# Kernel tuning notes

Measured on AMD Instinct MI355X. Metric: run time of the kernel, lower is better.

## Reference

```python
import jax, jax.numpy as jnp
import numpy as np

B, N, FIN, FOUT = 8, 1024, 512, 256
ALPHA = 0.2      # LeakyReLU negative slope
EPS = 1e-5       # LayerNorm eps
NEG = -9e15      # mask value


def setup_inputs() -> dict:
    key = jax.random.key(0)
    k_h, k_adj, k_W, k_a, k_g, k_b = jax.random.split(key, 6)
    h = jax.random.normal(k_h, (B, N, FIN), dtype=jnp.float32)
    # sparse-ish binary adjacency (float, as in the torch module: adj > 0 masks)
    adj = jax.random.bernoulli(k_adj, p=0.1, shape=(B, N, N)).astype(jnp.float32)
    # xavier_uniform with gain=1.414
    def xavier(k, shape, gain=1.414):
        fan_in, fan_out = shape[0], shape[1]
        lim = gain * np.sqrt(6.0 / (fan_in + fan_out))
        return jax.random.uniform(k, shape, jnp.float32, -lim, lim)
    W = xavier(k_W, (FIN, FOUT))
    a = xavier(k_a, (2 * FOUT, 1))
    ln_gamma = jnp.ones((FOUT,), jnp.float32)
    ln_beta = jnp.zeros((FOUT,), jnp.float32)
    return {"h": h, "adj": adj, "q_type": 0, "pos": 0,
            "W": W, "a": a, "ln_gamma": ln_gamma, "ln_beta": ln_beta}


def reference(h, adj, q_type, pos, W, a, ln_gamma, ln_beta):
    # h: [B,N,FIN], adj: [B,N,N]
    Wh = jnp.einsum('bnf,fo->bno', h, W)              # [B,N,FOUT]
    # a^T [Wh_i || Wh_j] decomposes into per-node terms (same math as the
    # torch repeat/cat construction, without the [B,N,N,2F] blowup)
    a1, a2 = a[:FOUT, 0], a[FOUT:, 0]                 # [FOUT], [FOUT]
    f1 = Wh @ a1                                      # [B,N] (source i)
    f2 = Wh @ a2                                      # [B,N] (target j)
    e = jax.nn.leaky_relu(f1[:, :, None] + f2[:, None, :], negative_slope=ALPHA)
    e = jnp.where(adj > 0, e, NEG)
    attention = jax.nn.softmax(e, axis=2)             # [B,N,N]
    # dropout is a no-op at inference (training=False)
    h_prime = jnp.einsum('bij,bjo->bio', attention, Wh)  # [B,N,FOUT]
    mu = jnp.mean(h_prime, axis=-1, keepdims=True)
    var = jnp.var(h_prime, axis=-1, keepdims=True)
    h_norm = (h_prime - mu) * jax.lax.rsqrt(var + EPS) * ln_gamma + ln_beta
    return jax.nn.gelu(h_norm, approximate=False)     # concat=True -> gelu
```

## Files before the change

kernel.cpp:

```cpp
#include <hip/hip_runtime.h>
#include <math.h>

#define B_    8
#define N_    1024
#define FIN   512
#define FOUT  256
#define ALPHA 0.2f
#define EPSV  1e-5f

typedef __attribute__((ext_vector_type(8))) short bf16x8;
typedef __attribute__((ext_vector_type(4))) float f32x4;

__device__ __forceinline__ short f2bf(float x) {
    unsigned u = __builtin_bit_cast(unsigned, x);
    u = (u + 0x7FFFu + ((u >> 16) & 1u)) >> 16;
    return (short)u;
}
__device__ __forceinline__ short f2bf_fast(float x) {
    unsigned u = __builtin_bit_cast(unsigned, x);
    return (short)((u + 0x8000u) >> 16);
}
__device__ __forceinline__ float bf2f(short s) {
    return __builtin_bit_cast(float, ((unsigned)(unsigned short)s) << 16);
}
__device__ __forceinline__ float gelu_exact(float x) {
    return 0.5f * x * (1.0f + erff(x * 0.70710678118654752f));
}


__global__ __launch_bounds__(256) void k_prep(const float* __restrict__ W,
                                              short* __restrict__ WT) {
    int id  = blockIdx.x * 256 + threadIdx.x;
    int col = id >> 7;
    int k4  = (id & 127) * 4;
    short4 v;
    v.x = f2bf(W[(k4 + 0) * FOUT + col]);
    v.y = f2bf(W[(k4 + 1) * FOUT + col]);
    v.z = f2bf(W[(k4 + 2) * FOUT + col]);
    v.w = f2bf(W[(k4 + 3) * FOUT + col]);
    *(short4*)(WT + (long)col * FIN + k4) = v;
}

__global__ __launch_bounds__(256) void k_bits(const float* __restrict__ adj,
                                              unsigned char* __restrict__ bits) {
    const int tid = threadIdx.x;
    const int w   = tid >> 6, l = tid & 63;
    const long gr = (long)blockIdx.x * 4 + w;
    const float* __restrict__ arow = adj + gr * N_;

    unsigned b0 = 0, b1 = 0;
    {
        float4 x0 = *(const float4*)(arow + l * 8);
        float4 x1 = *(const float4*)(arow + l * 8 + 4);
        float aa[8] = {x0.x, x0.y, x0.z, x0.w, x1.x, x1.y, x1.z, x1.w};
        #pragma unroll
        for (int u = 0; u < 8; ++u) b0 |= (aa[u] > 0.f ? 1u : 0u) << u;
        float4 y0 = *(const float4*)(arow + 512 + l * 8);
        float4 y1 = *(const float4*)(arow + 512 + l * 8 + 4);
        float bb[8] = {y0.x, y0.y, y0.z, y0.w, y1.x, y1.y, y1.z, y1.w};
        #pragma unroll
        for (int u = 0; u < 8; ++u) b1 |= (bb[u] > 0.f ? 1u : 0u) << u;
    }
    unsigned out2 = 0;
    #pragma unroll
    for (int k = 0; k < 2; ++k) {
        int o   = 2 * l + k;
        int lqd = o >> 5, ktd = o & 31;
        int src = ((ktd & 15) << 2) | lqd;
        unsigned v0 = __shfl(b0, src, 64);
        unsigned v1 = __shfl(b1, src, 64);
        unsigned v  = (ktd & 16) ? v1 : v0;
        out2 |= (v & 0xFFu) << (8 * k);
    }
    *(unsigned short*)(bits + gr * 128 + l * 2) = (unsigned short)out2;
}

__global__ __launch_bounds__(256) void k_wh(const float* __restrict__ h,
                                            const short* __restrict__ WT,
                                            const float* __restrict__ a,
                                            short* __restrict__ Bpack,
                                            float* __restrict__ F1,
                                            float* __restrict__ F2) {
    const int tid = threadIdx.x;
    const int w   = tid >> 6, l = tid & 63;
    const int lr  = l & 15, lq = l >> 4;
    const long row0 = (long)blockIdx.x * 16;
    const int colbase = w * 64;

    __shared__ float r1[4][16], r2[4][16];

    f32x4 acc[4] = {};
    const float* hrow = h + (row0 + lr) * FIN + lq * 8;

    #pragma unroll
    for (int k0 = 0; k0 < FIN; k0 += 32) {
        float4 v0 = *(const float4*)(hrow + k0);
        float4 v1 = *(const float4*)(hrow + k0 + 4);
        bf16x8 af;
        af[0] = f2bf(v0.x); af[1] = f2bf(v0.y); af[2] = f2bf(v0.z); af[3] = f2bf(v0.w);
        af[4] = f2bf(v1.x); af[5] = f2bf(v1.y); af[6] = f2bf(v1.z); af[7] = f2bf(v1.w);
        #pragma unroll
        for (int c = 0; c < 4; ++c) {
            const short* bp = WT + (long)(colbase + c * 16 + lr) * FIN + k0 + lq * 8;
            bf16x8 bf = *(const bf16x8*)bp;
            acc[c] = __builtin_amdgcn_mfma_f32_16x16x32_bf16(af, bf, acc[c], 0, 0, 0);
        }
    }

    const int b   = (int)(row0 >> 10);
    const int il0 = (int)(row0 & 1023);
    const int kt  = il0 >> 5;
    const int h16 = (il0 >> 4) & 1;
    const int lp  = (h16 * 2 + (lq >> 1)) * 16 + lr;
    const int u0  = (lq & 1) * 4;
    short* bpo = Bpack + ((long)b * 16 * 32) * 512;
    #pragma unroll
    for (int c = 0; c < 4; ++c) {
        short4 s;
        s.x = f2bf(acc[c][0]); s.y = f2bf(acc[c][1]);
        s.z = f2bf(acc[c][2]); s.w = f2bf(acc[c][3]);
        int n16 = w * 4 + c;
        *(short4*)(bpo + ((long)(n16 * 32 + kt)) * 512 + lp * 8 + u0) = s;
    }

    float p1[4] = {0.f, 0.f, 0.f, 0.f}, p2[4] = {0.f, 0.f, 0.f, 0.f};
    #pragma unroll
    for (int c = 0; c < 4; ++c) {
        int col = colbase + c * 16 + lr;
        float a1v = a[col], a2v = a[FOUT + col];
        #pragma unroll
        for (int j = 0; j < 4; ++j) { p1[j] += acc[c][j] * a1v; p2[j] += acc[c][j] * a2v; }
    }
    #pragma unroll
    for (int off = 1; off < 16; off <<= 1) {
        #pragma unroll
        for (int j = 0; j < 4; ++j) {
            p1[j] += __shfl_xor(p1[j], off, 64);
            p2[j] += __shfl_xor(p2[j], off, 64);
        }
    }
    if (lr == 0) {
        #pragma unroll
        for (int j = 0; j < 4; ++j) { r1[w][lq * 4 + j] = p1[j]; r2[w][lq * 4 + j] = p2[j]; }
    }
    __syncthreads();
    if (tid < 16) {
        F1[row0 + tid] = r1[0][tid] + r1[1][tid] + r1[2][tid] + r1[3][tid];
        F2[row0 + tid] = r2[0][tid] + r2[1][tid] + r2[2][tid] + r2[3][tid];
    }
}

__global__ __launch_bounds__(256) void k_pv(const short* __restrict__ Bpack,
                                            const unsigned char* __restrict__ bits,
                                            const float* __restrict__ F1,
                                            const float* __restrict__ F2,
                                            const float* __restrict__ gamma,
                                            const float* __restrict__ beta,
                                            float* __restrict__ out) {
    const int tid = threadIdx.x;
    const int b   = blockIdx.x;
    const int i0  = blockIdx.y * 16;
    const int w   = tid >> 6, l = tid & 63;
    const int lr  = l & 15, lq = l >> 4;

    __shared__ float f2s[N_];
    __shared__ float lnp1[4][16], lnp2[4][16];

    { int j = tid * 4; *(float4*)&f2s[j] = *(const float4*)(F2 + b * N_ + j); }
    __syncthreads();

    const float f1 = F1[b * N_ + i0 + lr];
    unsigned bw[8];
    {
        const unsigned char* pb = bits + ((long)(b * N_ + i0 + lr)) * 128 + lq * 32;
        uint4 q0 = *(const uint4*)pb;
        uint4 q1 = *(const uint4*)(pb + 16);
        bw[0]=q0.x; bw[1]=q0.y; bw[2]=q0.z; bw[3]=q0.w;
        bw[4]=q1.x; bw[5]=q1.y; bw[6]=q1.z; bw[7]=q1.w;
    }
    const short* __restrict__ bp = Bpack + (((long)b * 16 + w * 4) * 32) * 512 + l * 8;

    f32x4 acc[4] = {};
    float ls = 0.f;

    bf16x8 bc0 = *(const bf16x8*)(bp);
    bf16x8 bc1 = *(const bf16x8*)(bp + 32 * 512);
    bf16x8 bc2 = *(const bf16x8*)(bp + 64 * 512);
    bf16x8 bc3 = *(const bf16x8*)(bp + 96 * 512);

    #pragma unroll
    for (int t = 0; t < 32; ++t) {
        bf16x8 bn0 = bc0, bn1 = bc1, bn2 = bc2, bn3 = bc3;
        if (t < 31) {
            bn0 = *(const bf16x8*)(bp + (t + 1) * 512);
            bn1 = *(const bf16x8*)(bp + (32 + t + 1) * 512);
            bn2 = *(const bf16x8*)(bp + (64 + t + 1) * 512);
            bn3 = *(const bf16x8*)(bp + (96 + t + 1) * 512);
        }
        float f2k[8];
        *(float4*)&f2k[0] = *(const float4*)&f2s[t * 32 + lq * 8];
        *(float4*)&f2k[4] = *(const float4*)&f2s[t * 32 + lq * 8 + 4];
        const unsigned byte = (bw[t >> 2] >> ((t & 3) * 8)) & 0xFFu;

        bf16x8 af;
        #pragma unroll
        for (int u = 0; u < 8; ++u) {
            float x  = f1 + f2k[u];
            float tt = fmaxf(x, ALPHA * x);
            float e  = ((byte >> u) & 1u) ? __expf(tt) : 0.f;
            short s  = f2bf_fast(e);
            af[u] = s;
            ls += bf2f(s);
        }
        acc[0] = __builtin_amdgcn_mfma_f32_16x16x32_bf16(af, bc0, acc[0], 0, 0, 0);
        acc[1] = __builtin_amdgcn_mfma_f32_16x16x32_bf16(af, bc1, acc[1], 0, 0, 0);
        acc[2] = __builtin_amdgcn_mfma_f32_16x16x32_bf16(af, bc2, acc[2], 0, 0, 0);
        acc[3] = __builtin_amdgcn_mfma_f32_16x16x32_bf16(af, bc3, acc[3], 0, 0, 0);
        bc0 = bn0; bc1 = bn1; bc2 = bn2; bc3 = bn3;
    }

    ls += __shfl_xor(ls, 16, 64);
    ls += __shfl_xor(ls, 32, 64);
    float il[4];
    #pragma unroll
    for (int jj = 0; jj < 4; ++jj) {
        float r = __shfl(ls, lq * 4 + jj, 64);
        il[jj] = (r > 0.f) ? 1.0f / r : 0.f;
    }

    float s1[4] = {0.f,0.f,0.f,0.f}, s2[4] = {0.f,0.f,0.f,0.f};
    #pragma unroll
    for (int cf = 0; cf < 4; ++cf)
        #pragma unroll
        for (int jj = 0; jj < 4; ++jj) {
            float v = acc[cf][jj] * il[jj];
            acc[cf][jj] = v;
            s1[jj] += v;
            s2[jj] += v * v;
        }
    #pragma unroll
    for (int off = 1; off < 16; off <<= 1)
        #pragma unroll
        for (int jj = 0; jj < 4; ++jj) {
            s1[jj] += __shfl_xor(s1[jj], off, 64);
            s2[jj] += __shfl_xor(s2[jj], off, 64);
        }
    if (lr == 0) {
        #pragma unroll
        for (int jj = 0; jj < 4; ++jj) {
            lnp1[w][lq * 4 + jj] = s1[jj];
            lnp2[w][lq * 4 + jj] = s2[jj];
        }
    }
    __syncthreads();

    #pragma unroll
    for (int jj = 0; jj < 4; ++jj) {
        int row = lq * 4 + jj;
        float t1 = lnp1[0][row] + lnp1[1][row] + lnp1[2][row] + lnp1[3][row];
        float t2 = lnp2[0][row] + lnp2[1][row] + lnp2[2][row] + lnp2[3][row];
        float mu   = t1 * (1.0f / FOUT);
        float rstd = rsqrtf(t2 * (1.0f / FOUT) - mu * mu + EPSV);
        #pragma unroll
        for (int cf = 0; cf < 4; ++cf) {
            int col = w * 64 + cf * 16 + lr;
            out[((long)b * N_ + i0 + row) * FOUT + col] =
                gelu_exact((acc[cf][jj] - mu) * rstd * gamma[col] + beta[col]);
        }
    }
}

extern "C" void kernel_launch(void* const* d_in, const int* in_sizes, int n_in,
                              void* d_out, int out_size, void* d_ws, size_t ws_size,
                              hipStream_t stream) {
    const float* h     = (const float*)d_in[0];
    const float* adj   = (const float*)d_in[1];
    const float* W     = (const float*)d_in[4];
    const float* a     = (const float*)d_in[5];
    const float* gamma = (const float*)d_in[6];
    const float* beta  = (const float*)d_in[7];
    float* out = (float*)d_out;

    short* Bpack = (short*)d_ws;
    short* WT    = Bpack + (size_t)B_ * 16 * 32 * 512;
    float* F1    = (float*)(WT + (size_t)FOUT * FIN);
    float* F2    = F1 + (size_t)B_ * N_;
    unsigned char* bits = (unsigned char*)(F2 + (size_t)B_ * N_);

    k_prep<<<dim3(128), 256, 0, stream>>>(W, WT);
    k_bits<<<dim3(B_ * N_ / 4), 256, 0, stream>>>(adj, bits);
    k_wh  <<<dim3(B_ * N_ / 16), 256, 0, stream>>>(h, WT, a, Bpack, F1, F2);
    k_pv  <<<dim3(B_, N_ / 16), 256, 0, stream>>>(Bpack, bits, F1, F2, gamma, beta, out);
}
```

Before: 60.33 us.

## Split k_pv reduction dimension across two wave groups with LDS combine

Doubles the k_pv block to 512 threads so two groups of four waves each cover half of the key dimension. Partial accumulators and row sums are combined through shared memory before LayerNorm and GELU. The explicit software prefetch of B operands is dropped in favour of direct loads, leaving latency hiding to the extra waves. The intent is to halve the serial MFMA/exp chain per wave and raise occupancy. The cost is extra LDS traffic, another barrier, and half the waves idling during the epilogue.

```diff
diff --git a/kernel.cpp b/kernel.cpp
--- a/kernel.cpp
+++ b/kernel.cpp
@@ -150,56 +150,47 @@
     }
 }
 
-__global__ __launch_bounds__(256) void k_pv(const short* __restrict__ Bpack,
-                                            const unsigned char* __restrict__ bits,
-                                            const float* __restrict__ F1,
-                                            const float* __restrict__ F2,
-                                            const float* __restrict__ gamma,
-                                            const float* __restrict__ beta,
-                                            float* __restrict__ out) {
+__global__ __launch_bounds__(512, 4) void k_pv(const short* __restrict__ Bpack,
+                                               const unsigned char* __restrict__ bits,
+                                               const float* __restrict__ F1,
+                                               const float* __restrict__ F2,
+                                               const float* __restrict__ gamma,
+                                               const float* __restrict__ beta,
+                                               float* __restrict__ out) {
     const int tid = threadIdx.x;
     const int b   = blockIdx.x;
     const int i0  = blockIdx.y * 16;
     const int w   = tid >> 6, l = tid & 63;
     const int lr  = l & 15, lq = l >> 4;
+    const int cw  = w & 3;
+    const int kg  = w >> 2;
 
     __shared__ float f2s[N_];
+    __shared__ float sc[4][16][68];
     __shared__ float lnp1[4][16], lnp2[4][16];
-
-    { int j = tid * 4; *(float4*)&f2s[j] = *(const float4*)(F2 + b * N_ + j); }
+    __shared__ float lsumS[2][16];
+
+    { int j = tid * 2; *(float2*)&f2s[j] = *(const float2*)(F2 + b * N_ + j); }
     __syncthreads();
 
     const float f1 = F1[b * N_ + i0 + lr];
-    unsigned bw[8];
+    unsigned bw[4];
     {
-        const unsigned char* pb = bits + ((long)(b * N_ + i0 + lr)) * 128 + lq * 32;
-        uint4 q0 = *(const uint4*)pb;
-        uint4 q1 = *(const uint4*)(pb + 16);
-        bw[0]=q0.x; bw[1]=q0.y; bw[2]=q0.z; bw[3]=q0.w;
-        bw[4]=q1.x; bw[5]=q1.y; bw[6]=q1.z; bw[7]=q1.w;
-    }
-    const short* __restrict__ bp = Bpack + (((long)b * 16 + w * 4) * 32) * 512 + l * 8;
+        const unsigned char* pb = bits + ((long)(b * N_ + i0 + lr)) * 128 + lq * 32 + kg * 16;
+        uint4 q = *(const uint4*)pb;
+        bw[0] = q.x; bw[1] = q.y; bw[2] = q.z; bw[3] = q.w;
+    }
+    const short* __restrict__ bp =
+        Bpack + (((long)b * 16 + cw * 4) * 32 + kg * 16) * 512 + l * 8;
 
     f32x4 acc[4] = {};
     float ls = 0.f;
 
-    bf16x8 bc0 = *(const bf16x8*)(bp);
-    bf16x8 bc1 = *(const bf16x8*)(bp + 32 * 512);
-    bf16x8 bc2 = *(const bf16x8*)(bp + 64 * 512);
-    bf16x8 bc3 = *(const bf16x8*)(bp + 96 * 512);
-
-    #pragma unroll
-    for (int t = 0; t < 32; ++t) {
-        bf16x8 bn0 = bc0, bn1 = bc1, bn2 = bc2, bn3 = bc3;
-        if (t < 31) {
-            bn0 = *(const bf16x8*)(bp + (t + 1) * 512);
-            bn1 = *(const bf16x8*)(bp + (32 + t + 1) * 512);
-            bn2 = *(const bf16x8*)(bp + (64 + t + 1) * 512);
-            bn3 = *(const bf16x8*)(bp + (96 + t + 1) * 512);
-        }
+    #pragma unroll
+    for (int t = 0; t < 16; ++t) {
         float f2k[8];
-        *(float4*)&f2k[0] = *(const float4*)&f2s[t * 32 + lq * 8];
-        *(float4*)&f2k[4] = *(const float4*)&f2s[t * 32 + lq * 8 + 4];
+        *(float4*)&f2k[0] = *(const float4*)&f2s[(kg * 16 + t) * 32 + lq * 8];
+        *(float4*)&f2k[4] = *(const float4*)&f2s[(kg * 16 + t) * 32 + lq * 8 + 4];
         const unsigned byte = (bw[t >> 2] >> ((t & 3) * 8)) & 0xFFu;
 
         bf16x8 af;
@@ -212,60 +203,83 @@
             af[u] = s;
             ls += bf2f(s);
         }
-        acc[0] = __builtin_amdgcn_mfma_f32_16x16x32_bf16(af, bc0, acc[0], 0, 0, 0);
-        acc[1] = __builtin_amdgcn_mfma_f32_16x16x32_bf16(af, bc1, acc[1], 0, 0, 0);
-        acc[2] = __builtin_amdgcn_mfma_f32_16x16x32_bf16(af, bc2, acc[2], 0, 0, 0);
-        acc[3] = __builtin_amdgcn_mfma_f32_16x16x32_bf16(af, bc3, acc[3], 0, 0, 0);
-        bc0 = bn0; bc1 = bn1; bc2 = bn2; bc3 = bn3;
+        bf16x8 b0 = *(const bf16x8*)(bp + (long)t * 512);
+        bf16x8 b1 = *(const bf16x8*)(bp + (long)(32 + t) * 512);
+        bf16x8 b2 = *(const bf16x8*)(bp + (long)(64 + t) * 512);
+        bf16x8 b3 = *(const bf16x8*)(bp + (long)(96 + t) * 512);
+        acc[0] = __builtin_amdgcn_mfma_f32_16x16x32_bf16(af, b0, acc[0], 0, 0, 0);
+        acc[1] = __builtin_amdgcn_mfma_f32_16x16x32_bf16(af, b1, acc[1], 0, 0, 0);
+        acc[2] = __builtin_amdgcn_mfma_f32_16x16x32_bf16(af, b2, acc[2], 0, 0, 0);
+        acc[3] = __builtin_amdgcn_mfma_f32_16x16x32_bf16(af, b3, acc[3], 0, 0, 0);
     }
 
     ls += __shfl_xor(ls, 16, 64);
     ls += __shfl_xor(ls, 32, 64);
-    float il[4];
-    #pragma unroll
-    for (int jj = 0; jj < 4; ++jj) {
-        float r = __shfl(ls, lq * 4 + jj, 64);
-        il[jj] = (r > 0.f) ? 1.0f / r : 0.f;
-    }
-
-    float s1[4] = {0.f,0.f,0.f,0.f}, s2[4] = {0.f,0.f,0.f,0.f};
-    #pragma unroll
-    for (int cf = 0; cf < 4; ++cf)
+    if (cw == 0 && lq == 0) lsumS[kg][lr] = ls;
+
+    if (kg == 1) {
+        #pragma unroll
+        for (int cf = 0; cf < 4; ++cf)
+            #pragma unroll
+            for (int jj = 0; jj < 4; ++jj)
+                sc[cw][lq * 4 + jj][cf * 16 + lr] = acc[cf][jj];
+    }
+    __syncthreads();
+
+    if (kg == 0) {
+        #pragma unroll
+        for (int cf = 0; cf < 4; ++cf)
+            #pragma unroll
+            for (int jj = 0; jj < 4; ++jj)
+                acc[cf][jj] += sc[cw][lq * 4 + jj][cf * 16 + lr];
+
+        float il[4];
         #pragma unroll
         for (int jj = 0; jj < 4; ++jj) {
-            float v = acc[cf][jj] * il[jj];
-            acc[cf][jj] = v;
-            s1[jj] += v;
-            s2[jj] += v * v;
-        }
-    #pragma unroll
-    for (int off = 1; off < 16; off <<= 1)
+            float r = lsumS[0][lq * 4 + jj] + lsumS[1][lq * 4 + jj];
+            il[jj] = (r > 0.f) ? 1.0f / r : 0.f;
+        }
+        float s1[4] = {0.f,0.f,0.f,0.f}, s2[4] = {0.f,0.f,0.f,0.f};
+        #pragma unroll
+        for (int cf = 0; cf < 4; ++cf)
+            #pragma unroll
+            for (int jj = 0; jj < 4; ++jj) {
+                float v = acc[cf][jj] * il[jj];
+                acc[cf][jj] = v;
+                s1[jj] += v;
+                s2[jj] += v * v;
+            }
+        #pragma unroll
+        for (int off = 1; off < 16; off <<= 1)
+            #pragma unroll
+            for (int jj = 0; jj < 4; ++jj) {
+                s1[jj] += __shfl_xor(s1[jj], off, 64);
+                s2[jj] += __shfl_xor(s2[jj], off, 64);
+            }
+        if (lr == 0) {
+            #pragma unroll
+            for (int jj = 0; jj < 4; ++jj) {
+                lnp1[cw][lq * 4 + jj] = s1[jj];
+                lnp2[cw][lq * 4 + jj] = s2[jj];
+            }
+        }
+    }
+    __syncthreads();
+
+    if (kg == 0) {
         #pragma unroll
         for (int jj = 0; jj < 4; ++jj) {
-            s1[jj] += __shfl_xor(s1[jj], off, 64);
-            s2[jj] += __shfl_xor(s2[jj], off, 64);
-        }
-    if (lr == 0) {
-        #pragma unroll
-        for (int jj = 0; jj < 4; ++jj) {
-            lnp1[w][lq * 4 + jj] = s1[jj];
-            lnp2[w][lq * 4 + jj] = s2[jj];
-        }
-    }
-    __syncthreads();
-
-    #pragma unroll
-    for (int jj = 0; jj < 4; ++jj) {
-        int row = lq * 4 + jj;
-        float t1 = lnp1[0][row] + lnp1[1][row] + lnp1[2][row] + lnp1[3][row];
-        float t2 = lnp2[0][row] + lnp2[1][row] + lnp2[2][row] + lnp2[3][row];
-        float mu   = t1 * (1.0f / FOUT);
-        float rstd = rsqrtf(t2 * (1.0f / FOUT) - mu * mu + EPSV);
-        #pragma unroll
-        for (int cf = 0; cf < 4; ++cf) {
-            int col = w * 64 + cf * 16 + lr;
-            out[((long)b * N_ + i0 + row) * FOUT + col] =
-                gelu_exact((acc[cf][jj] - mu) * rstd * gamma[col] + beta[col]);
+            int row = lq * 4 + jj;
+            float t1 = lnp1[0][row] + lnp1[1][row] + lnp1[2][row] + lnp1[3][row];
+            float t2 = lnp2[0][row] + lnp2[1][row] + lnp2[2][row] + lnp2[3][row];
+            float mu   = t1 * (1.0f / FOUT);
+            float rstd = rsqrtf(t2 * (1.0f / FOUT) - mu * mu + EPSV);
+            #pragma unroll
+            for (int cf = 0; cf < 4; ++cf) {
+                int col = cw * 64 + cf * 16 + lr;
+                out[((long)b * N_ + i0 + row) * FOUT + col] =
+                    gelu_exact((acc[cf][jj] - mu) * rstd * gamma[col] + beta[col]);
+            }
         }
     }
 }
@@ -290,5 +304,5 @@
     k_prep<<<dim3(128), 256, 0, stream>>>(W, WT);
     k_bits<<<dim3(B_ * N_ / 4), 256, 0, stream>>>(adj, bits);
     k_wh  <<<dim3(B_ * N_ / 16), 256, 0, stream>>>(h, WT, a, Bpack, F1, F2);
-    k_pv  <<<dim3(B_, N_ / 16), 256, 0, stream>>>(Bpack, bits, F1, F2, gamma, beta, out);
-}
+    k_pv  <<<dim3(B_, N_ / 16), 512, 0, stream>>>(Bpack, bits, F1, F2, gamma, beta, out);
+}
```

Measured after the change: 60.43 us. No clear change (+0.2%).

## Split attention into prob-gen, LDS-staged MFMA GEMM, and separate LayerNorm kernels

Applied to the files above, without the earlier changes.

The fused attention kernel is split into three kernels. k_pgen materializes the masked exp scores as packed bf16 A tiles plus row sums. k_pv is a double-buffered GEMM that stages A and B tiles into LDS with global_load_lds and computes 32x128 output tiles. k_ln then applies the softmax normalization, LayerNorm and GELU in place. The aim is more reuse of Wh tiles across rows and better MFMA throughput, at the cost of writing and re-reading a 16MB bf16 probability matrix and the fp32 intermediate, plus two extra launches.

```diff
diff --git a/kernel.cpp b/kernel.cpp
--- a/kernel.cpp
+++ b/kernel.cpp
@@ -150,124 +150,169 @@
     }
 }
 
-__global__ __launch_bounds__(256) void k_pv(const short* __restrict__ Bpack,
-                                            const unsigned char* __restrict__ bits,
-                                            const float* __restrict__ F1,
-                                            const float* __restrict__ F2,
-                                            const float* __restrict__ gamma,
-                                            const float* __restrict__ beta,
-                                            float* __restrict__ out) {
+__global__ __launch_bounds__(256) void k_pgen(const unsigned char* __restrict__ bits,
+                                              const float* __restrict__ F1,
+                                              const float* __restrict__ F2,
+                                              short* __restrict__ Apack,
+                                              float* __restrict__ lrow) {
     const int tid = threadIdx.x;
     const int b   = blockIdx.x;
-    const int i0  = blockIdx.y * 16;
+    const int m16 = blockIdx.y;
+    const int i0  = m16 * 16;
     const int w   = tid >> 6, l = tid & 63;
     const int lr  = l & 15, lq = l >> 4;
 
     __shared__ float f2s[N_];
-    __shared__ float lnp1[4][16], lnp2[4][16];
-
+    __shared__ float lred[4][16];
     { int j = tid * 4; *(float4*)&f2s[j] = *(const float4*)(F2 + b * N_ + j); }
     __syncthreads();
 
     const float f1 = F1[b * N_ + i0 + lr];
-    unsigned bw[8];
-    {
-        const unsigned char* pb = bits + ((long)(b * N_ + i0 + lr)) * 128 + lq * 32;
-        uint4 q0 = *(const uint4*)pb;
-        uint4 q1 = *(const uint4*)(pb + 16);
-        bw[0]=q0.x; bw[1]=q0.y; bw[2]=q0.z; bw[3]=q0.w;
-        bw[4]=q1.x; bw[5]=q1.y; bw[6]=q1.z; bw[7]=q1.w;
-    }
-    const short* __restrict__ bp = Bpack + (((long)b * 16 + w * 4) * 32) * 512 + l * 8;
-
-    f32x4 acc[4] = {};
+    const uint2 bw2 = *(const uint2*)(bits + ((long)(b * N_ + i0 + lr)) * 128 + lq * 32 + w * 8);
+    const unsigned bwv[2] = {bw2.x, bw2.y};
+    short* __restrict__ apb = Apack + (((long)b * 64 + m16) * 32) * 512;
+
     float ls = 0.f;
-
-    bf16x8 bc0 = *(const bf16x8*)(bp);
-    bf16x8 bc1 = *(const bf16x8*)(bp + 32 * 512);
-    bf16x8 bc2 = *(const bf16x8*)(bp + 64 * 512);
-    bf16x8 bc3 = *(const bf16x8*)(bp + 96 * 512);
-
-    #pragma unroll
-    for (int t = 0; t < 32; ++t) {
-        bf16x8 bn0 = bc0, bn1 = bc1, bn2 = bc2, bn3 = bc3;
-        if (t < 31) {
-            bn0 = *(const bf16x8*)(bp + (t + 1) * 512);
-            bn1 = *(const bf16x8*)(bp + (32 + t + 1) * 512);
-            bn2 = *(const bf16x8*)(bp + (64 + t + 1) * 512);
-            bn3 = *(const bf16x8*)(bp + (96 + t + 1) * 512);
-        }
+    #pragma unroll
+    for (int it = 0; it < 8; ++it) {
+        const int kt = w * 8 + it;
+        const unsigned byte = (bwv[it >> 2] >> ((it & 3) * 8)) & 0xFFu;
         float f2k[8];
-        *(float4*)&f2k[0] = *(const float4*)&f2s[t * 32 + lq * 8];
-        *(float4*)&f2k[4] = *(const float4*)&f2s[t * 32 + lq * 8 + 4];
-        const unsigned byte = (bw[t >> 2] >> ((t & 3) * 8)) & 0xFFu;
-
-        bf16x8 af;
+        *(float4*)&f2k[0] = *(const float4*)&f2s[kt * 32 + lq * 8];
+        *(float4*)&f2k[4] = *(const float4*)&f2s[kt * 32 + lq * 8 + 4];
+        bf16x8 pv;
         #pragma unroll
         for (int u = 0; u < 8; ++u) {
             float x  = f1 + f2k[u];
             float tt = fmaxf(x, ALPHA * x);
             float e  = ((byte >> u) & 1u) ? __expf(tt) : 0.f;
             short s  = f2bf_fast(e);
-            af[u] = s;
+            pv[u] = s;
             ls += bf2f(s);
         }
-        acc[0] = __builtin_amdgcn_mfma_f32_16x16x32_bf16(af, bc0, acc[0], 0, 0, 0);
-        acc[1] = __builtin_amdgcn_mfma_f32_16x16x32_bf16(af, bc1, acc[1], 0, 0, 0);
-        acc[2] = __builtin_amdgcn_mfma_f32_16x16x32_bf16(af, bc2, acc[2], 0, 0, 0);
-        acc[3] = __builtin_amdgcn_mfma_f32_16x16x32_bf16(af, bc3, acc[3], 0, 0, 0);
-        bc0 = bn0; bc1 = bn1; bc2 = bn2; bc3 = bn3;
+        *(bf16x8*)(apb + (long)kt * 512 + l * 8) = pv;
     }
 
     ls += __shfl_xor(ls, 16, 64);
     ls += __shfl_xor(ls, 32, 64);
-    float il[4];
-    #pragma unroll
-    for (int jj = 0; jj < 4; ++jj) {
-        float r = __shfl(ls, lq * 4 + jj, 64);
-        il[jj] = (r > 0.f) ? 1.0f / r : 0.f;
-    }
-
-    float s1[4] = {0.f,0.f,0.f,0.f}, s2[4] = {0.f,0.f,0.f,0.f};
-    #pragma unroll
-    for (int cf = 0; cf < 4; ++cf)
-        #pragma unroll
-        for (int jj = 0; jj < 4; ++jj) {
-            float v = acc[cf][jj] * il[jj];
-            acc[cf][jj] = v;
-            s1[jj] += v;
-            s2[jj] += v * v;
-        }
-    #pragma unroll
-    for (int off = 1; off < 16; off <<= 1)
-        #pragma unroll
-        for (int jj = 0; jj < 4; ++jj) {
-            s1[jj] += __shfl_xor(s1[jj], off, 64);
-            s2[jj] += __shfl_xor(s2[jj], off, 64);
-        }
-    if (lr == 0) {
-        #pragma unroll
-        for (int jj = 0; jj < 4; ++jj) {
-            lnp1[w][lq * 4 + jj] = s1[jj];
-            lnp2[w][lq * 4 + jj] = s2[jj];
-        }
-    }
+    if (lq == 0) lred[w][lr] = ls;
     __syncthreads();
-
-    #pragma unroll
-    for (int jj = 0; jj < 4; ++jj) {
-        int row = lq * 4 + jj;
-        float t1 = lnp1[0][row] + lnp1[1][row] + lnp1[2][row] + lnp1[3][row];
-        float t2 = lnp2[0][row] + lnp2[1][row] + lnp2[2][row] + lnp2[3][row];
-        float mu   = t1 * (1.0f / FOUT);
-        float rstd = rsqrtf(t2 * (1.0f / FOUT) - mu * mu + EPSV);
-        #pragma unroll
-        for (int cf = 0; cf < 4; ++cf) {
-            int col = w * 64 + cf * 16 + lr;
-            out[((long)b * N_ + i0 + row) * FOUT + col] =
-                gelu_exact((acc[cf][jj] - mu) * rstd * gamma[col] + beta[col]);
-        }
-    }
+    if (tid < 16)
+        lrow[(long)b * N_ + i0 + tid] = lred[0][tid] + lred[1][tid] + lred[2][tid] + lred[3][tid];
+}
+
+__global__ __launch_bounds__(128) void k_pv(const short* __restrict__ Apack,
+                                            const short* __restrict__ Bpack,
+                                            float* __restrict__ hp) {
+    const int tid = threadIdx.x;
+    const int w   = tid >> 6, l = tid & 63;
+    const int lr  = l & 15, lq = l >> 4;
+    const int rg  = ((blockIdx.x & 7) << 5) | (blockIdx.x >> 3);
+    const int b   = rg >> 5;
+    const int rloc= rg & 31;
+    const int cg  = blockIdx.y;
+
+    __shared__ short sbuf[2][20 * 512];
+
+    const short* __restrict__ abase = Apack + (((long)b * 64 + rloc * 2) * 32) * 512 + (long)l * 8;
+    const short* __restrict__ bbase = Bpack + (((long)b * 16 + cg * 8) * 32) * 512 + (long)l * 8;
+
+    f32x4 acc[2][4] = {};
+
+    auto stage = [&](int buf, int t) {
+        const int kt0 = t * 2;
+        #pragma unroll
+        for (int c = w; c < 20; c += 2) {
+            const short* src;
+            if (c < 4) {
+                src = abase + ((long)(c >> 1) * 32 + kt0 + (c & 1)) * 512;
+            } else {
+                int idx = c - 4;
+                src = bbase + ((long)(idx >> 1) * 32 + kt0 + (idx & 1)) * 512;
+            }
+            __builtin_amdgcn_global_load_lds(
+                (const __attribute__((address_space(1))) unsigned int*)src,
+                (__attribute__((address_space(3))) unsigned int*)&sbuf[buf][c * 512],
+                16, 0, 0);
+        }
+    };
+
+    auto compute = [&](int buf) {
+        #pragma unroll
+        for (int kt2 = 0; kt2 < 2; ++kt2) {
+            bf16x8 a0 = *(const bf16x8*)&sbuf[buf][(0 + kt2) * 512 + l * 8];
+            bf16x8 a1 = *(const bf16x8*)&sbuf[buf][(2 + kt2) * 512 + l * 8];
+            #pragma unroll
+            for (int cf = 0; cf < 4; ++cf) {
+                const int n = w * 4 + cf;
+                bf16x8 bv = *(const bf16x8*)&sbuf[buf][(4 + n * 2 + kt2) * 512 + l * 8];
+                acc[0][cf] = __builtin_amdgcn_mfma_f32_16x16x32_bf16(a0, bv, acc[0][cf], 0, 0, 0);
+                acc[1][cf] = __builtin_amdgcn_mfma_f32_16x16x32_bf16(a1, bv, acc[1][cf], 0, 0, 0);
+            }
+        }
+    };
+
+    stage(0, 0);
+    __syncthreads();
+    int cur = 0;
+    for (int t = 0; t < 16; ++t) {
+        if (t < 15) stage(cur ^ 1, t + 1);
+        compute(cur);
+        __syncthreads();
+        cur ^= 1;
+    }
+
+    const long row0 = (long)b * 1024 + (long)rloc * 32;
+    const int  c0   = cg * 128 + w * 64;
+    #pragma unroll
+    for (int rf = 0; rf < 2; ++rf)
+        #pragma unroll
+        for (int cf = 0; cf < 4; ++cf)
+            #pragma unroll
+            for (int jj = 0; jj < 4; ++jj)
+                hp[(row0 + rf * 16 + lq * 4 + jj) * FOUT + c0 + cf * 16 + lr] = acc[rf][cf][jj];
+}
+
+__global__ __launch_bounds__(256) void k_ln(float* __restrict__ hp,
+                                            const float* __restrict__ lrow,
+                                            const float* __restrict__ gamma,
+                                            const float* __restrict__ beta) {
+    const int tid = threadIdx.x;
+    const long row = (long)blockIdx.x * 8 + (tid >> 5);
+    const int sub = tid & 31, f0 = sub * 8;
+
+    float* p = hp + row * FOUT + f0;
+    float4 v0 = *(const float4*)p;
+    float4 v1 = *(const float4*)(p + 4);
+    float lv = lrow[row];
+    float il = (lv > 0.f) ? 1.0f / lv : 0.f;
+    float v[8] = {v0.x, v0.y, v0.z, v0.w, v1.x, v1.y, v1.z, v1.w};
+    float s1 = 0.f, s2 = 0.f;
+    #pragma unroll
+    for (int u = 0; u < 8; ++u) { v[u] *= il; s1 += v[u]; s2 += v[u] * v[u]; }
+    #pragma unroll
+    for (int off = 1; off < 32; off <<= 1) {
+        s1 += __shfl_xor(s1, off, 64);
+        s2 += __shfl_xor(s2, off, 64);
+    }
+    const float mu   = s1 * (1.0f / FOUT);
+    const float rstd = rsqrtf(s2 * (1.0f / FOUT) - mu * mu + EPSV);
+
+    float4 g0 = *(const float4*)(gamma + f0);
+    float4 g1 = *(const float4*)(gamma + f0 + 4);
+    float4 b0 = *(const float4*)(beta + f0);
+    float4 b1 = *(const float4*)(beta + f0 + 4);
+    float4 o0, o1;
+    o0.x = gelu_exact((v[0] - mu) * rstd * g0.x + b0.x);
+    o0.y = gelu_exact((v[1] - mu) * rstd * g0.y + b0.y);
+    o0.z = gelu_exact((v[2] - mu) * rstd * g0.z + b0.z);
+    o0.w = gelu_exact((v[3] - mu) * rstd * g0.w + b0.w);
+    o1.x = gelu_exact((v[4] - mu) * rstd * g1.x + b1.x);
+    o1.y = gelu_exact((v[5] - mu) * rstd * g1.y + b1.y);
+    o1.z = gelu_exact((v[6] - mu) * rstd * g1.z + b1.z);
+    o1.w = gelu_exact((v[7] - mu) * rstd * g1.w + b1.w);
+    *(float4*)p       = o0;
+    *(float4*)(p + 4) = o1;
 }
 
 extern "C" void kernel_launch(void* const* d_in, const int* in_sizes, int n_in,
@@ -281,14 +326,18 @@
     const float* beta  = (const float*)d_in[7];
     float* out = (float*)d_out;
 
-    short* Bpack = (short*)d_ws;
+    short* Apack = (short*)d_ws;
+    short* Bpack = Apack + (size_t)B_ * 64 * 32 * 512;
     short* WT    = Bpack + (size_t)B_ * 16 * 32 * 512;
     float* F1    = (float*)(WT + (size_t)FOUT * FIN);
     float* F2    = F1 + (size_t)B_ * N_;
     unsigned char* bits = (unsigned char*)(F2 + (size_t)B_ * N_);
+    float* lrow  = (float*)(bits + (size_t)B_ * N_ * 128);
 
     k_prep<<<dim3(128), 256, 0, stream>>>(W, WT);
     k_bits<<<dim3(B_ * N_ / 4), 256, 0, stream>>>(adj, bits);
     k_wh  <<<dim3(B_ * N_ / 16), 256, 0, stream>>>(h, WT, a, Bpack, F1, F2);
-    k_pv  <<<dim3(B_, N_ / 16), 256, 0, stream>>>(Bpack, bits, F1, F2, gamma, beta, out);
-}
+    k_pgen<<<dim3(B_, N_ / 16), 256, 0, stream>>>(bits, F1, F2, Apack, lrow);
+    k_pv  <<<dim3(256, 2), 128, 0, stream>>>(Apack, Bpack, out);
+    k_ln  <<<dim3(B_ * N_ / 8), 256, 0, stream>>>(out, lrow, gamma, beta);
+}
```

After: 68.47 us. 13.5% more time.
